# Kernel optimization log

Measured on AMD Instinct MI355X. Metric: run time of the kernel, lower is better.

The kernel has to match this reference:

```python
import jax, jax.numpy as jnp
import numpy as np

B, S, D = 8, 2048, 512
LN_EPS = 1e-5

def _layernorm(x, gamma, beta):
    mu = jnp.mean(x, axis=-1, keepdims=True)
    var = jnp.mean(jnp.square(x - mu), axis=-1, keepdims=True)
    return (x - mu) * jax.lax.rsqrt(var + LN_EPS) * gamma + beta

def setup_inputs() -> dict:
    key = jax.random.key(0)
    ks = jax.random.split(key, 10)
    s_in = 1.0 / np.sqrt(2 * D)
    s_d = 1.0 / np.sqrt(D)
    return {
        "Noise_x": jax.random.normal(ks[0], (B, S, D), jnp.float32),
        "X": jax.random.normal(ks[1], (B, S, D), jnp.float32),
        "cond": jax.random.normal(ks[2], (B, S, D), jnp.float32),
        "W_gate": jax.random.normal(ks[3], (2 * D, D), jnp.float32) * s_in,
        "b_gate": jnp.zeros((D,), jnp.float32),
        "W1": jax.random.normal(ks[4], (D, 2 * D), jnp.float32) * s_d,
        "b1": jnp.zeros((2 * D,), jnp.float32),
        "W2": jax.random.normal(ks[5], (2 * D, D), jnp.float32) * s_in,
        "b2": jnp.zeros((D,), jnp.float32),
        "g1": jnp.ones((D,), jnp.float32),
        "be1": jnp.zeros((D,), jnp.float32),
        "g2": jnp.ones((D,), jnp.float32),
        "be2": jnp.zeros((D,), jnp.float32),
    }

def reference(Noise_x, X, cond, W_gate, b_gate, W1, b1, W2, b2, g1, be1, g2, be2):
    # gated fusion of noise and condition
    combined = jnp.concatenate([Noise_x, cond], axis=-1)            # [B,S,2D]
    gate = jax.nn.sigmoid(combined @ W_gate + b_gate)               # [B,S,D]
    fused = gate * Noise_x + (1.0 - gate) * cond                    # [B,S,D]
    # hand-rolled attention: Q = fused, K = V = X
    scale = 1.0 / jnp.sqrt(jnp.asarray(D, fused.dtype))
    scores = jnp.einsum('bqd,bkd->bqk', fused, X) * scale           # [B,S,S]
    attn = jax.nn.softmax(scores, axis=-1)
    attn_out = jnp.einsum('bqk,bkd->bqd', attn, X)                  # [B,S,D]
    # residual + norm, FFN (exact GELU as in torch default), residual + norm
    q = _layernorm(fused + attn_out, g1, be1)
    ff = jax.nn.gelu(q @ W1 + b1, approximate=False) @ W2 + b2
    return _layernorm(q + ff, g2, be2)
```

## Files before the change

### kernel.cpp

```cpp
#include <hip/hip_runtime.h>
#include <math.h>

typedef unsigned short ushort_t;
typedef unsigned int uint_t;
typedef __attribute__((ext_vector_type(8))) short short8;
typedef __attribute__((ext_vector_type(4))) float floatx4;

constexpr int B = 8;
constexpr int S = 2048;
constexpr int D = 512;
constexpr int BS = B * S;
constexpr float LN_EPS = 1e-5f;
constexpr float ATTN_SCALE = 0.04419417382415922f;


__device__ __forceinline__ ushort_t f2bf(float f) {
    union { float f; uint_t u; } x; x.f = f;
    uint_t r = x.u + 0x7fffu + ((x.u >> 16) & 1u);
    return (ushort_t)(r >> 16);
}
__device__ __forceinline__ float bf2f(ushort_t h) {
    union { uint_t u; float f; } y; y.u = ((uint_t)h) << 16;
    return y.f;
}
__device__ __forceinline__ short8 pack8(float4 a, float4 b) {
    short8 p;
    p[0] = (short)f2bf(a.x); p[1] = (short)f2bf(a.y);
    p[2] = (short)f2bf(a.z); p[3] = (short)f2bf(a.w);
    p[4] = (short)f2bf(b.x); p[5] = (short)f2bf(b.y);
    p[6] = (short)f2bf(b.z); p[7] = (short)f2bf(b.w);
    return p;
}

__device__ __forceinline__ float blk_reduce_sum(float v, float* sm) {
#pragma unroll
    for (int o = 32; o; o >>= 1) v += __shfl_down(v, o, 64);
    __syncthreads();
    if ((threadIdx.x & 63) == 0) sm[threadIdx.x >> 6] = v;
    __syncthreads();
    return sm[0] + sm[1] + sm[2] + sm[3];
}
__device__ __forceinline__ float blk_reduce_max(float v, float* sm) {
#pragma unroll
    for (int o = 32; o; o >>= 1) v = fmaxf(v, __shfl_down(v, o, 64));
    __syncthreads();
    if ((threadIdx.x & 63) == 0) sm[threadIdx.x >> 6] = v;
    __syncthreads();
    return fmaxf(fmaxf(sm[0], sm[1]), fmaxf(sm[2], sm[3]));
}

__global__ __launch_bounds__(256) void transpose_cvt(
    const float* __restrict__ in, ushort_t* __restrict__ out, int R, int C,
    ushort_t* __restrict__ out2) {
    __shared__ float tl[32][33];
    const size_t zoff = (size_t)blockIdx.z * R * C;
    const int tx = threadIdx.x & 31, ty = threadIdx.x >> 5;
    const int c0 = blockIdx.x * 32, r0 = blockIdx.y * 32;
#pragma unroll
    for (int i = 0; i < 4; i++) {
        const float v = in[zoff + (size_t)(r0 + ty + i * 8) * C + c0 + tx];
        tl[ty + i * 8][tx] = v;
        if (out2) out2[zoff + (size_t)(r0 + ty + i * 8) * C + c0 + tx] = f2bf(v);
    }
    __syncthreads();
#pragma unroll
    for (int i = 0; i < 4; i++)
        out[zoff + (size_t)(c0 + ty + i * 8) * R + r0 + tx] = f2bf(tl[tx][ty + i * 8]);
}

#define IDX128()                                                               \
    const int t = threadIdx.x;                                                 \
    const int sr = t >> 2;                                          \
    const int sc = (t & 3) * 8;                                 \
    const int lane = t & 63, w = t >> 6;                                       \
    const int fr = lane & 15, fq = lane >> 4;

#define MFMA16(Asp, Bsp)                                                       \
    {                                                                          \
        short8 af[4], bfg[4];                                                  \
        _Pragma("unroll") for (int i = 0; i < 4; i++) {                        \
            af[i]  = *(const short8*)&(Asp)[(wm + i * 16 + fr) * 40 + fq * 8]; \
            bfg[i] = *(const short8*)&(Bsp)[(wn + i * 16 + fr) * 40 + fq * 8]; \
        }                                                                      \
        _Pragma("unroll") for (int i = 0; i < 4; i++)                          \
            _Pragma("unroll") for (int j = 0; j < 4; j++)                      \
                acc[i][j] = __builtin_amdgcn_mfma_f32_16x16x32_bf16(           \
                    af[i], bfg[j], acc[i][j], 0, 0, 0);                        \
    }

#define MFMA8(Asp, Bsp)                                                        \
    {                                                                          \
        short8 af[2], bfg[4];                                                  \
        _Pragma("unroll") for (int i = 0; i < 2; i++)                          \
            af[i]  = *(const short8*)&(Asp)[(wm + i * 16 + fr) * 40 + fq * 8]; \
        _Pragma("unroll") for (int j = 0; j < 4; j++)                          \
            bfg[j] = *(const short8*)&(Bsp)[(j * 16 + fr) * 40 + fq * 8];      \
        _Pragma("unroll") for (int i = 0; i < 2; i++)                          \
            _Pragma("unroll") for (int j = 0; j < 4; j++)                      \
                acc[i][j] = __builtin_amdgcn_mfma_f32_16x16x32_bf16(           \
                    af[i], bfg[j], acc[i][j], 0, 0, 0);                        \
    }

__global__ __launch_bounds__(256) void gate_gemm(
    const float* __restrict__ NX, const float* __restrict__ CD,
    const ushort_t* __restrict__ WgT, const float* __restrict__ bg,
    ushort_t* __restrict__ Fb) {
    __shared__ ushort_t As[2][128 * 40];
    __shared__ ushort_t Bs[2][128 * 40];
    IDX128();
    const int m0 = blockIdx.y * 128, n0 = blockIdx.x * 128;
    const int wm = (w >> 1) * 64, wn = (w & 1) * 64;
    floatx4 acc[4][4];
#pragma unroll
    for (int i = 0; i < 4; i++)
#pragma unroll
        for (int j = 0; j < 4; j++) {
            acc[i][j][0] = 0.f; acc[i][j][1] = 0.f;
            acc[i][j][2] = 0.f; acc[i][j][3] = 0.f;
        }
    const ushort_t* Bb = WgT + (size_t)n0 * 1024;

    float4 f00, f01, f10, f11;
    int4 b0, b1;
    {
        const float* p0 = NX + (size_t)(m0 + sr) * 512 + sc;
        const float* p1 = NX + (size_t)(m0 + sr + 64) * 512 + sc;
        f00 = *(const float4*)p0;  f01 = *(const float4*)(p0 + 4);
        f10 = *(const float4*)p1;  f11 = *(const float4*)(p1 + 4);
        b0 = *(const int4*)(Bb + (size_t)sr * 1024 + sc);
        b1 = *(const int4*)(Bb + (size_t)(sr + 64) * 1024 + sc);
        *(short8*)&As[0][sr * 40 + sc] = pack8(f00, f01);
        *(short8*)&As[0][(sr + 64) * 40 + sc] = pack8(f10, f11);
        *(int4*)&Bs[0][sr * 40 + sc] = b0;
        *(int4*)&Bs[0][(sr + 64) * 40 + sc] = b1;
    }
    {
        const float* p0 = NX + (size_t)(m0 + sr) * 512 + 32 + sc;
        const float* p1 = NX + (size_t)(m0 + sr + 64) * 512 + 32 + sc;
        f00 = *(const float4*)p0;  f01 = *(const float4*)(p0 + 4);
        f10 = *(const float4*)p1;  f11 = *(const float4*)(p1 + 4);
        b0 = *(const int4*)(Bb + (size_t)sr * 1024 + 32 + sc);
        b1 = *(const int4*)(Bb + (size_t)(sr + 64) * 1024 + 32 + sc);
    }
    __syncthreads();

    int cur = 0;
    for (int k0 = 0; k0 < 1024; k0 += 32) {
        MFMA16(As[cur], Bs[cur]);
        const int kn = k0 + 32;
        if (kn < 1024) {
            *(short8*)&As[cur ^ 1][sr * 40 + sc] = pack8(f00, f01);
            *(short8*)&As[cur ^ 1][(sr + 64) * 40 + sc] = pack8(f10, f11);
            *(int4*)&Bs[cur ^ 1][sr * 40 + sc] = b0;
            *(int4*)&Bs[cur ^ 1][(sr + 64) * 40 + sc] = b1;
            const int kf = kn + 32;
            if (kf < 1024) {
                const float* Asrc = (kf < 512) ? NX : CD;
                const int kk = kf & 511;
                const float* p0 = Asrc + (size_t)(m0 + sr) * 512 + kk + sc;
                const float* p1 = Asrc + (size_t)(m0 + sr + 64) * 512 + kk + sc;
                f00 = *(const float4*)p0;  f01 = *(const float4*)(p0 + 4);
                f10 = *(const float4*)p1;  f11 = *(const float4*)(p1 + 4);
                b0 = *(const int4*)(Bb + (size_t)sr * 1024 + kf + sc);
                b1 = *(const int4*)(Bb + (size_t)(sr + 64) * 1024 + kf + sc);
            }
        }
        __syncthreads();
        cur ^= 1;
    }

#pragma unroll
    for (int i = 0; i < 4; i++) {
#pragma unroll
        for (int j = 0; j < 4; j++) {
#pragma unroll
            for (int r = 0; r < 4; r++) {
                const int m = m0 + wm + i * 16 + fq * 4 + r;
                const int n = n0 + wn + j * 16 + fr;
                const float z = acc[i][j][r] + bg[n];
                const float g = 1.f / (1.f + expf(-z));
                const size_t idx = (size_t)m * 512 + n;
                Fb[idx] = f2bf(g * NX[idx] + (1.f - g) * CD[idx]);
            }
        }
    }
}

template <int EPI>
__global__ __launch_bounds__(256) void gemm2_std(
    const ushort_t* __restrict__ A, int lda, long sAz,
    const ushort_t* __restrict__ Bt, int ldb, long sBz,
    void* __restrict__ Cv, int ldc, long sCz,
    int K, const float* __restrict__ bias, float scale, int init) {
    __shared__ ushort_t As[2][128 * 40];
    __shared__ ushort_t Bs[2][128 * 40];
    IDX128();
    const int m0 = blockIdx.y * 128, n0 = blockIdx.x * 128;
    const int wm = (w >> 1) * 64, wn = (w & 1) * 64;
    floatx4 acc[4][4];
#pragma unroll
    for (int i = 0; i < 4; i++)
#pragma unroll
        for (int j = 0; j < 4; j++) {
            acc[i][j][0] = 0.f; acc[i][j][1] = 0.f;
            acc[i][j][2] = 0.f; acc[i][j][3] = 0.f;
        }
    const ushort_t* Ab = A + (size_t)blockIdx.z * sAz + (size_t)m0 * lda;
    const ushort_t* Bb = Bt + (size_t)blockIdx.z * sBz + (size_t)n0 * ldb;

    int4 a0 = *(const int4*)(Ab + (size_t)sr * lda + sc);
    int4 a1 = *(const int4*)(Ab + (size_t)(sr + 64) * lda + sc);
    int4 b0 = *(const int4*)(Bb + (size_t)sr * ldb + sc);
    int4 b1 = *(const int4*)(Bb + (size_t)(sr + 64) * ldb + sc);
    *(int4*)&As[0][sr * 40 + sc] = a0;
    *(int4*)&As[0][(sr + 64) * 40 + sc] = a1;
    *(int4*)&Bs[0][sr * 40 + sc] = b0;
    *(int4*)&Bs[0][(sr + 64) * 40 + sc] = b1;
    if (32 < K) {
        a0 = *(const int4*)(Ab + (size_t)sr * lda + 32 + sc);
        a1 = *(const int4*)(Ab + (size_t)(sr + 64) * lda + 32 + sc);
        b0 = *(const int4*)(Bb + (size_t)sr * ldb + 32 + sc);
        b1 = *(const int4*)(Bb + (size_t)(sr + 64) * ldb + 32 + sc);
    }
    __syncthreads();

    int cur = 0;
    for (int k0 = 0; k0 < K; k0 += 32) {
        MFMA16(As[cur], Bs[cur]);
        const int kn = k0 + 32;
        if (kn < K) {
            *(int4*)&As[cur ^ 1][sr * 40 + sc] = a0;
            *(int4*)&As[cur ^ 1][(sr + 64) * 40 + sc] = a1;
            *(int4*)&Bs[cur ^ 1][sr * 40 + sc] = b0;
            *(int4*)&Bs[cur ^ 1][(sr + 64) * 40 + sc] = b1;
            const int kf = kn + 32;
            if (kf < K) {
                a0 = *(const int4*)(Ab + (size_t)sr * lda + kf + sc);
                a1 = *(const int4*)(Ab + (size_t)(sr + 64) * lda + kf + sc);
                b0 = *(const int4*)(Bb + (size_t)sr * ldb + kf + sc);
                b1 = *(const int4*)(Bb + (size_t)(sr + 64) * ldb + kf + sc);
            }
        }
        __syncthreads();
        cur ^= 1;
    }

#pragma unroll
    for (int i = 0; i < 4; i++) {
#pragma unroll
        for (int j = 0; j < 4; j++) {
#pragma unroll
            for (int r = 0; r < 4; r++) {
                const int m = m0 + wm + i * 16 + fq * 4 + r;
                const int n = n0 + wn + j * 16 + fr;
                float v = acc[i][j][r];
                if (EPI == 0) {
                    ushort_t* C = (ushort_t*)Cv + (size_t)blockIdx.z * sCz;
                    C[(size_t)m * ldc + n] = f2bf(v * scale);
                } else if (EPI == 1) {
                    const float x = v + bias[n];
                    const float gl = 0.5f * x * (1.f + erff(x * 0.70710678118654752f));
                    ushort_t* C = (ushort_t*)Cv;
                    C[(size_t)m * ldc + n] = f2bf(gl);
                } else {
                    float* T = (float*)Cv;
                    const size_t idx = (size_t)m * ldc + n;
                    T[idx] = T[idx] + v + (init ? bias[n] : 0.f);
                }
            }
        }
    }
}

template <int EPI>
__global__ __launch_bounds__(256) void gemm3_std(
    const ushort_t* __restrict__ A, int lda, long sAz,
    const ushort_t* __restrict__ Bt, int ldb, long sBz,
    void* __restrict__ Cv, int ldc, long sCz,
    int K, const float* __restrict__ bias, float scale, int init) {
    __shared__ ushort_t As[2][128 * 40];
    __shared__ ushort_t Bs[2][64 * 40];
    IDX128();
    const int m0 = blockIdx.y * 128, n0 = blockIdx.x * 64;
    const int wm = w * 32;
    floatx4 acc[2][4];
#pragma unroll
    for (int i = 0; i < 2; i++)
#pragma unroll
        for (int j = 0; j < 4; j++) {
            acc[i][j][0] = 0.f; acc[i][j][1] = 0.f;
            acc[i][j][2] = 0.f; acc[i][j][3] = 0.f;
        }
    const ushort_t* Ab = A + (size_t)blockIdx.z * sAz + (size_t)m0 * lda;
    const ushort_t* Bb = Bt + (size_t)blockIdx.z * sBz + (size_t)n0 * ldb;

    int4 a0 = *(const int4*)(Ab + (size_t)sr * lda + sc);
    int4 a1 = *(const int4*)(Ab + (size_t)(sr + 64) * lda + sc);
    int4 b0 = *(const int4*)(Bb + (size_t)sr * ldb + sc);
    *(int4*)&As[0][sr * 40 + sc] = a0;
    *(int4*)&As[0][(sr + 64) * 40 + sc] = a1;
    *(int4*)&Bs[0][sr * 40 + sc] = b0;
    if (32 < K) {
        a0 = *(const int4*)(Ab + (size_t)sr * lda + 32 + sc);
        a1 = *(const int4*)(Ab + (size_t)(sr + 64) * lda + 32 + sc);
        b0 = *(const int4*)(Bb + (size_t)sr * ldb + 32 + sc);
    }
    __syncthreads();

    int cur = 0;
    for (int k0 = 0; k0 < K; k0 += 32) {
        MFMA8(As[cur], Bs[cur]);
        const int kn = k0 + 32;
        if (kn < K) {
            *(int4*)&As[cur ^ 1][sr * 40 + sc] = a0;
            *(int4*)&As[cur ^ 1][(sr + 64) * 40 + sc] = a1;
            *(int4*)&Bs[cur ^ 1][sr * 40 + sc] = b0;
            const int kf = kn + 32;
            if (kf < K) {
                a0 = *(const int4*)(Ab + (size_t)sr * lda + kf + sc);
                a1 = *(const int4*)(Ab + (size_t)(sr + 64) * lda + kf + sc);
                b0 = *(const int4*)(Bb + (size_t)sr * ldb + kf + sc);
            }
        }
        __syncthreads();
        cur ^= 1;
    }

#pragma unroll
    for (int i = 0; i < 2; i++) {
#pragma unroll
        for (int j = 0; j < 4; j++) {
#pragma unroll
            for (int r = 0; r < 4; r++) {
                const int m = m0 + wm + i * 16 + fq * 4 + r;
                const int n = n0 + j * 16 + fr;
                float v = acc[i][j][r];
                if (EPI == 0) {
                    ushort_t* C = (ushort_t*)Cv + (size_t)blockIdx.z * sCz;
                    C[(size_t)m * ldc + n] = f2bf(v * scale);
                } else if (EPI == 1) {
                    const float x = v + bias[n];
                    const float gl = 0.5f * x * (1.f + erff(x * 0.70710678118654752f));
                    ushort_t* C = (ushort_t*)Cv;
                    C[(size_t)m * ldc + n] = f2bf(gl);
                } else {
                    float* T = (float*)Cv;
                    const size_t idx = (size_t)m * ldc + n;
                    T[idx] = T[idx] + v + (init ? bias[n] : 0.f);
                }
            }
        }
    }
}

__global__ __launch_bounds__(256) void softmax_bf16(ushort_t* __restrict__ Sc) {
    __shared__ float sm[4];
    ushort_t* row = Sc + (size_t)blockIdx.x * 2048;
    const int t = threadIdx.x;
    ushort_t raw[8];
    *(int4*)raw = *(const int4*)(row + t * 8);
    float e[8];
    float mx = -1e30f;
#pragma unroll
    for (int j = 0; j < 8; j++) { e[j] = bf2f(raw[j]); mx = fmaxf(mx, e[j]); }
    mx = blk_reduce_max(mx, sm);
    float s = 0.f;
#pragma unroll
    for (int j = 0; j < 8; j++) { e[j] = expf(e[j] - mx); s += e[j]; }
    s = blk_reduce_sum(s, sm);
    const float inv = 1.f / s;
#pragma unroll
    for (int j = 0; j < 8; j++) raw[j] = f2bf(e[j] * inv);
    *(int4*)(row + t * 8) = *(const int4*)raw;
}

__global__ __launch_bounds__(256) void ln1_kernel(
    const ushort_t* __restrict__ Fb, const ushort_t* __restrict__ Ab,
    const float* __restrict__ g1, const float* __restrict__ be1,
    float* __restrict__ qf, ushort_t* __restrict__ qb) {
    __shared__ float sm[4];
    const size_t base = (size_t)blockIdx.x * 512;
    const int t = threadIdx.x;
    const float v0 = bf2f(Fb[base + t]) + bf2f(Ab[base + t]);
    const float v1 = bf2f(Fb[base + t + 256]) + bf2f(Ab[base + t + 256]);
    const float mu = blk_reduce_sum(v0 + v1, sm) * (1.f / 512.f);
    const float d0 = v0 - mu, d1 = v1 - mu;
    const float var = blk_reduce_sum(d0 * d0 + d1 * d1, sm) * (1.f / 512.f);
    const float rs = rsqrtf(var + LN_EPS);
    const float y0 = d0 * rs * g1[t] + be1[t];
    const float y1 = d1 * rs * g1[t + 256] + be1[t + 256];
    qf[base + t] = y0;          qf[base + t + 256] = y1;
    qb[base + t] = f2bf(y0);    qb[base + t + 256] = f2bf(y1);
}

__global__ __launch_bounds__(256) void ln2_kernel(
    float* __restrict__ T, const float* __restrict__ g,
    const float* __restrict__ be) {
    __shared__ float sm[4];
    const size_t base = (size_t)blockIdx.x * 512;
    const int t = threadIdx.x;
    const float v0 = T[base + t];
    const float v1 = T[base + t + 256];
    const float mu = blk_reduce_sum(v0 + v1, sm) * (1.f / 512.f);
    const float d0 = v0 - mu, d1 = v1 - mu;
    const float var = blk_reduce_sum(d0 * d0 + d1 * d1, sm) * (1.f / 512.f);
    const float rs = rsqrtf(var + LN_EPS);
    T[base + t] = d0 * rs * g[t] + be[t];
    T[base + t + 256] = d1 * rs * g[t + 256] + be[t + 256];
}

extern "C" void kernel_launch(void* const* d_in, const int* in_sizes, int n_in,
                              void* d_out, int out_size, void* d_ws, size_t ws_size,
                              hipStream_t stream) {
    const float* NX  = (const float*)d_in[0];
    const float* X   = (const float*)d_in[1];
    const float* CD  = (const float*)d_in[2];
    const float* Wg  = (const float*)d_in[3];
    const float* bg  = (const float*)d_in[4];
    const float* W1  = (const float*)d_in[5];
    const float* b1  = (const float*)d_in[6];
    const float* W2  = (const float*)d_in[7];
    const float* b2  = (const float*)d_in[8];
    const float* g1  = (const float*)d_in[9];
    const float* be1 = (const float*)d_in[10];
    const float* g2  = (const float*)d_in[11];
    const float* be2 = (const float*)d_in[12];

    ushort_t* slot0 = (ushort_t*)d_ws;
    ushort_t* slot1 = (ushort_t*)((char*)d_ws + 16777216);
    ushort_t* slot2 = (ushort_t*)((char*)d_ws + 33554432);
    ushort_t* Xb    = slot0;
    ushort_t* attnb = slot0;
    ushort_t* hbuf  = slot0;
    ushort_t* Fb    = slot1;
    ushort_t* W1T   = slot1;
    ushort_t* W2T   = slot1 + 524288;
    ushort_t* WgT   = slot2;
    ushort_t* XbT   = slot2;
    ushort_t* qb    = slot2;
    ushort_t* Scb   = (ushort_t*)d_out;
    float*    qf    = (float*)d_out;

    transpose_cvt<<<dim3(512 / 32, 1024 / 32, 1), 256, 0, stream>>>(
        Wg, WgT, 1024, 512, nullptr);

    gate_gemm<<<dim3(4, 128), 256, 0, stream>>>(NX, CD, WgT, bg, Fb);

    transpose_cvt<<<dim3(512 / 32, 2048 / 32, 8), 256, 0, stream>>>(
        X, XbT, 2048, 512, Xb);

    for (int g = 0; g < 2; g++) {
        const size_t go = (size_t)g * 4 * S * 512;
        gemm2_std<0><<<dim3(16, 16, 4), 256, 0, stream>>>(
            Fb + go, D, (long)S * D,
            Xb + go, D, (long)S * D,
            (void*)Scb, S, (long)S * S, D, nullptr, ATTN_SCALE, 0);
        softmax_bf16<<<4 * S, 256, 0, stream>>>(Scb);
        gemm3_std<0><<<dim3(8, 16, 4), 256, 0, stream>>>(
            Scb, S, (long)S * S,
            XbT + go, S, (long)D * S,
            (void*)(attnb + go), 512, (long)S * 512, S, nullptr, 1.f, 0);
    }

    ln1_kernel<<<BS, 256, 0, stream>>>(Fb, attnb, g1, be1, qf, qb);

    transpose_cvt<<<dim3(1024 / 32, 512 / 32, 1), 256, 0, stream>>>(
        W1, W1T, 512, 1024, nullptr);
    transpose_cvt<<<dim3(512 / 32, 1024 / 32, 1), 256, 0, stream>>>(
        W2, W2T, 1024, 512, nullptr);

    for (int h = 0; h < 2; h++) {
        gemm2_std<1><<<dim3(4, 128), 256, 0, stream>>>(
            qb, 512, 0, W1T + (size_t)h * 512 * 512, 512, 0,
            (void*)hbuf, 512, 0, 512, b1 + h * 512, 1.f, 0);
        gemm2_std<2><<<dim3(4, 128), 256, 0, stream>>>(
            hbuf, 512, 0, W2T + h * 512, 1024, 0,
            (void*)qf, 512, 0, 512, b2, 1.f, h == 0 ? 1 : 0);
    }

    ln2_kernel<<<BS, 256, 0, stream>>>(qf, g2, be2);
}
```

Before: 539.0 us.

## Swizzle workgroup order across XCDs and deepen gemm3 K-tile to 64

Adds a block-index remapping that groups consecutive logical tiles onto the same XCD (stride-8 interleave), applied to gate_gemm, gemm2_std and gemm3_std, to improve L2 locality for shared A/B tiles. gemm3_std also switches from a 32-wide to a 64-wide K step with padded 72-element rows, halving the number of barriers and loop iterations per tile. The cost is larger LDS usage and more staging registers, which could lower occupancy, and the swizzle assumes the total workgroup count divides evenly by 8.

```diff
diff --git a/kernel.cpp b/kernel.cpp
--- a/kernel.cpp
+++ b/kernel.cpp
@@ -31,6 +31,19 @@
     p[6] = (short)f2bf(b.z); p[7] = (short)f2bf(b.w);
     return p;
 }
+
+#define SWZ_DECODE(bx, by, bz)                                                 \
+    int bx, by, bz;                                                            \
+    {                                                                          \
+        const int gx = gridDim.x, gy = gridDim.y;                              \
+        const int nwg = gx * gy * (int)gridDim.z;                              \
+        const int F = blockIdx.x + gx * (blockIdx.y + gy * blockIdx.z);        \
+        const int L = (F & 7) * (nwg >> 3) + (F >> 3);                         \
+        bx = L % gx;                                                           \
+        const int l2 = L / gx;                                                 \
+        by = l2 % gy;                                                          \
+        bz = l2 / gy;                                                          \
+    }
 
 __device__ __forceinline__ float blk_reduce_sum(float v, float* sm) {
 #pragma unroll
@@ -88,27 +101,16 @@
                     af[i], bfg[j], acc[i][j], 0, 0, 0);                        \
     }
 
-#define MFMA8(Asp, Bsp)                                                        \
-    {                                                                          \
-        short8 af[2], bfg[4];                                                  \
-        _Pragma("unroll") for (int i = 0; i < 2; i++)                          \
-            af[i]  = *(const short8*)&(Asp)[(wm + i * 16 + fr) * 40 + fq * 8]; \
-        _Pragma("unroll") for (int j = 0; j < 4; j++)                          \
-            bfg[j] = *(const short8*)&(Bsp)[(j * 16 + fr) * 40 + fq * 8];      \
-        _Pragma("unroll") for (int i = 0; i < 2; i++)                          \
-            _Pragma("unroll") for (int j = 0; j < 4; j++)                      \
-                acc[i][j] = __builtin_amdgcn_mfma_f32_16x16x32_bf16(           \
-                    af[i], bfg[j], acc[i][j], 0, 0, 0);                        \
-    }
-
 __global__ __launch_bounds__(256) void gate_gemm(
     const float* __restrict__ NX, const float* __restrict__ CD,
     const ushort_t* __restrict__ WgT, const float* __restrict__ bg,
     ushort_t* __restrict__ Fb) {
     __shared__ ushort_t As[2][128 * 40];
     __shared__ ushort_t Bs[2][128 * 40];
+    SWZ_DECODE(bx, by, bz);
+    (void)bz;
     IDX128();
-    const int m0 = blockIdx.y * 128, n0 = blockIdx.x * 128;
+    const int m0 = by * 128, n0 = bx * 128;
     const int wm = (w >> 1) * 64, wn = (w & 1) * 64;
     floatx4 acc[4][4];
 #pragma unroll
@@ -194,8 +196,9 @@
     int K, const float* __restrict__ bias, float scale, int init) {
     __shared__ ushort_t As[2][128 * 40];
     __shared__ ushort_t Bs[2][128 * 40];
+    SWZ_DECODE(bx, by, bz);
     IDX128();
-    const int m0 = blockIdx.y * 128, n0 = blockIdx.x * 128;
+    const int m0 = by * 128, n0 = bx * 128;
     const int wm = (w >> 1) * 64, wn = (w & 1) * 64;
     floatx4 acc[4][4];
 #pragma unroll
@@ -205,8 +208,8 @@
             acc[i][j][0] = 0.f; acc[i][j][1] = 0.f;
             acc[i][j][2] = 0.f; acc[i][j][3] = 0.f;
         }
-    const ushort_t* Ab = A + (size_t)blockIdx.z * sAz + (size_t)m0 * lda;
-    const ushort_t* Bb = Bt + (size_t)blockIdx.z * sBz + (size_t)n0 * ldb;
+    const ushort_t* Ab = A + (size_t)bz * sAz + (size_t)m0 * lda;
+    const ushort_t* Bb = Bt + (size_t)bz * sBz + (size_t)n0 * ldb;
 
     int4 a0 = *(const int4*)(Ab + (size_t)sr * lda + sc);
     int4 a1 = *(const int4*)(Ab + (size_t)(sr + 64) * lda + sc);
@@ -255,7 +258,7 @@
                 const int n = n0 + wn + j * 16 + fr;
                 float v = acc[i][j][r];
                 if (EPI == 0) {
-                    ushort_t* C = (ushort_t*)Cv + (size_t)blockIdx.z * sCz;
+                    ushort_t* C = (ushort_t*)Cv + (size_t)bz * sCz;
                     C[(size_t)m * ldc + n] = f2bf(v * scale);
                 } else if (EPI == 1) {
                     const float x = v + bias[n];
@@ -278,11 +281,16 @@
     const ushort_t* __restrict__ Bt, int ldb, long sBz,
     void* __restrict__ Cv, int ldc, long sCz,
     int K, const float* __restrict__ bias, float scale, int init) {
-    __shared__ ushort_t As[2][128 * 40];
-    __shared__ ushort_t Bs[2][64 * 40];
-    IDX128();
-    const int m0 = blockIdx.y * 128, n0 = blockIdx.x * 64;
+    __shared__ ushort_t As[2][128 * 72];
+    __shared__ ushort_t Bs[2][64 * 72];
+    SWZ_DECODE(bx, by, bz);
+    const int t = threadIdx.x;
+    const int sr8 = t >> 3;
+    const int sc8 = (t & 7) * 8;
+    const int lane = t & 63, w = t >> 6;
     const int wm = w * 32;
+    const int fr = lane & 15, fq = lane >> 4;
+    const int m0 = by * 128, n0 = bx * 64;
     floatx4 acc[2][4];
 #pragma unroll
     for (int i = 0; i < 2; i++)
@@ -291,36 +299,52 @@
             acc[i][j][0] = 0.f; acc[i][j][1] = 0.f;
             acc[i][j][2] = 0.f; acc[i][j][3] = 0.f;
         }
-    const ushort_t* Ab = A + (size_t)blockIdx.z * sAz + (size_t)m0 * lda;
-    const ushort_t* Bb = Bt + (size_t)blockIdx.z * sBz + (size_t)n0 * ldb;
-
-    int4 a0 = *(const int4*)(Ab + (size_t)sr * lda + sc);
-    int4 a1 = *(const int4*)(Ab + (size_t)(sr + 64) * lda + sc);
-    int4 b0 = *(const int4*)(Bb + (size_t)sr * ldb + sc);
-    *(int4*)&As[0][sr * 40 + sc] = a0;
-    *(int4*)&As[0][(sr + 64) * 40 + sc] = a1;
-    *(int4*)&Bs[0][sr * 40 + sc] = b0;
-    if (32 < K) {
-        a0 = *(const int4*)(Ab + (size_t)sr * lda + 32 + sc);
-        a1 = *(const int4*)(Ab + (size_t)(sr + 64) * lda + 32 + sc);
-        b0 = *(const int4*)(Bb + (size_t)sr * ldb + 32 + sc);
-    }
+    const ushort_t* Ab = A + (size_t)bz * sAz + (size_t)m0 * lda;
+    const ushort_t* Bb = Bt + (size_t)bz * sBz + (size_t)n0 * ldb;
+
+    int4 ra[4], rb[2];
+#define G3_LD(k)                                                               \
+    {                                                                          \
+        _Pragma("unroll") for (int i = 0; i < 4; i++)                          \
+            ra[i] = *(const int4*)(Ab + (size_t)(sr8 + i * 32) * lda + (k) + sc8); \
+        _Pragma("unroll") for (int i = 0; i < 2; i++)                          \
+            rb[i] = *(const int4*)(Bb + (size_t)(sr8 + i * 32) * ldb + (k) + sc8); \
+    }
+#define G3_ST(buf)                                                             \
+    {                                                                          \
+        _Pragma("unroll") for (int i = 0; i < 4; i++)                          \
+            *(int4*)&As[buf][(sr8 + i * 32) * 72 + sc8] = ra[i];               \
+        _Pragma("unroll") for (int i = 0; i < 2; i++)                          \
+            *(int4*)&Bs[buf][(sr8 + i * 32) * 72 + sc8] = rb[i];               \
+    }
+
+    G3_LD(0);
+    G3_ST(0);
+    if (64 < K) G3_LD(64);
     __syncthreads();
 
     int cur = 0;
-    for (int k0 = 0; k0 < K; k0 += 32) {
-        MFMA8(As[cur], Bs[cur]);
-        const int kn = k0 + 32;
+    for (int k0 = 0; k0 < K; k0 += 64) {
+#pragma unroll
+        for (int kk = 0; kk < 2; kk++) {
+            short8 af[2], bfg[4];
+#pragma unroll
+            for (int i = 0; i < 2; i++)
+                af[i] = *(const short8*)&As[cur][(wm + i * 16 + fr) * 72 + kk * 32 + fq * 8];
+#pragma unroll
+            for (int j = 0; j < 4; j++)
+                bfg[j] = *(const short8*)&Bs[cur][(j * 16 + fr) * 72 + kk * 32 + fq * 8];
+#pragma unroll
+            for (int i = 0; i < 2; i++)
+#pragma unroll
+                for (int j = 0; j < 4; j++)
+                    acc[i][j] = __builtin_amdgcn_mfma_f32_16x16x32_bf16(
+                        af[i], bfg[j], acc[i][j], 0, 0, 0);
+        }
+        const int kn = k0 + 64;
         if (kn < K) {
-            *(int4*)&As[cur ^ 1][sr * 40 + sc] = a0;
-            *(int4*)&As[cur ^ 1][(sr + 64) * 40 + sc] = a1;
-            *(int4*)&Bs[cur ^ 1][sr * 40 + sc] = b0;
-            const int kf = kn + 32;
-            if (kf < K) {
-                a0 = *(const int4*)(Ab + (size_t)sr * lda + kf + sc);
-                a1 = *(const int4*)(Ab + (size_t)(sr + 64) * lda + kf + sc);
-                b0 = *(const int4*)(Bb + (size_t)sr * ldb + kf + sc);
-            }
+            G3_ST(cur ^ 1);
+            if (kn + 64 < K) G3_LD(kn + 64);
         }
         __syncthreads();
         cur ^= 1;
@@ -336,7 +360,7 @@
                 const int n = n0 + j * 16 + fr;
                 float v = acc[i][j][r];
                 if (EPI == 0) {
-                    ushort_t* C = (ushort_t*)Cv + (size_t)blockIdx.z * sCz;
+                    ushort_t* C = (ushort_t*)Cv + (size_t)bz * sCz;
                     C[(size_t)m * ldc + n] = f2bf(v * scale);
                 } else if (EPI == 1) {
                     const float x = v + bias[n];
@@ -351,6 +375,8 @@
             }
         }
     }
+#undef G3_LD
+#undef G3_ST
 }
 
 __global__ __launch_bounds__(256) void softmax_bf16(ushort_t* __restrict__ Sc) {
```

New measurement: 602.9 us. +11.9%, slower.
